# Optimization experiments

Hardware: AMD Instinct MI355X
Metric: run time of the kernel (lower is better)

## Reference

```python
import jax, jax.numpy as jnp
import numpy as np


def setup_inputs() -> dict:
    key = jax.random.key(0)
    k1, k2, k3, k4, k5 = jax.random.split(key, 5)
    B, C, D = 16384, 1000, 2048
    x = jax.random.normal(k1, (B, D), dtype=jnp.float32)
    W = jax.random.normal(k2, (C, D), dtype=jnp.float32) * 0.02  # fc weight
    b = jax.random.normal(k3, (C,), dtype=jnp.float32) * 0.01
    selector_weights = jax.random.normal(k4, (5,), dtype=jnp.float32) * 0.01
    selector_thresholds = jax.random.normal(k5, (5,), dtype=jnp.float32) * 0.01
    ensemble_threshold = jnp.zeros((1,), dtype=jnp.float32)
    return {
        "x": x, "W": W, "b": b,
        "selector_weights": selector_weights,
        "selector_thresholds": selector_thresholds,
        "ensemble_threshold": ensemble_threshold,
    }


def _selector_scores(logits, W):
    # top-2 of raw logits (RLConfM): sorted descending -> top_k(2)
    top2, _ = jax.lax.top_k(logits, 2)
    conf_m = top2[:, 0] - top2[:, 1]
    # geometric margin (RLGeoM): logits normalized by row norms of fc weight
    w_norms = jnp.linalg.norm(W, axis=1)                      # [C]
    norm_logits = logits / (w_norms + 1e-8)[None, :]          # [B, C]
    ntop2, _ = jax.lax.top_k(norm_logits, 2)
    geo_m = ntop2[:, 0] - ntop2[:, 1]
    # softmax-based selectors share one softmax pass
    probs = jax.nn.softmax(logits, axis=1)                    # [B, C]
    sr_max = jnp.max(probs, axis=1)
    doctor = 1.0 - 1.0 / jnp.sum(probs * probs, axis=1)
    neg_entropy = jnp.sum(probs * jnp.log(probs + 1e-10), axis=1)  # = -entropy
    # order matches nn.ModuleList: [SRMax, SRDoctor, SREntropy, RLGeoM, RLConfM]
    return jnp.stack([sr_max, doctor, neg_entropy, geo_m, conf_m], axis=1)  # [B, 5]


def reference(x, W, b, selector_weights, selector_thresholds, ensemble_threshold):
    # base model runs under no_grad in the original
    logits = jax.lax.stop_gradient(jnp.dot(x, W.T) + b)       # [B, C]
    scores = _selector_scores(logits, jax.lax.stop_gradient(W))  # [B, 5]
    indicators = jnp.tanh(scores - selector_thresholds[None, :])  # [B, 5]
    ensemble = jnp.sum(selector_weights[None, :] * indicators, axis=1)  # [B]
    selection_score = jnp.tanh(ensemble - ensemble_threshold[0])
    return (logits, selection_score)
```

## Files before the change

### kernel.cpp

```cpp
#include <hip/hip_runtime.h>
#include <stdint.h>

#define B_ROWS 16384
#define C_COLS 1000
#define D_DIM  2048

typedef __bf16 bf16x8 __attribute__((ext_vector_type(8)));
typedef float  f32x4  __attribute__((ext_vector_type(4)));
typedef unsigned short u16;

__device__ __forceinline__ u16 f2bf(float f) {
  union { float f; uint32_t u; } v; v.f = f;
  return (u16)((v.u + 0x7FFFu + ((v.u >> 16) & 1u)) >> 16);
}

__global__ __launch_bounds__(256)
void prep(const float* __restrict__ W, const float* __restrict__ x,
          u16* __restrict__ Wb, u16* __restrict__ xb, float* __restrict__ norms) {
  const int r = blockIdx.x;
  const int t = threadIdx.x;
  const bool isW = (r < C_COLS);
  const float* src = isW ? (W + (size_t)r * D_DIM)
                         : (x + (size_t)(r - C_COLS) * D_DIM);
  u16* dst = isW ? (Wb + (size_t)r * D_DIM)
                 : (xb + (size_t)(r - C_COLS) * D_DIM);
  const int c = t * 8;
  float4 v0 = *reinterpret_cast<const float4*>(src + c);
  float4 v1 = *reinterpret_cast<const float4*>(src + c + 4);
  uint32_t p0 = (uint32_t)f2bf(v0.x) | ((uint32_t)f2bf(v0.y) << 16);
  uint32_t p1 = (uint32_t)f2bf(v0.z) | ((uint32_t)f2bf(v0.w) << 16);
  uint32_t p2 = (uint32_t)f2bf(v1.x) | ((uint32_t)f2bf(v1.y) << 16);
  uint32_t p3 = (uint32_t)f2bf(v1.z) | ((uint32_t)f2bf(v1.w) << 16);
  const int mask = (r & 7) << 3;
  const int row_id = isW ? r : (r - C_COLS);
  const int m2 = (row_id & 7) << 3;
  (void)mask;
  uint4 val; val.x = p0; val.y = p1; val.z = p2; val.w = p3;
  *reinterpret_cast<uint4*>(dst + (c ^ m2)) = val;
  if (isW) {
    float ss = v0.x*v0.x + v0.y*v0.y + v0.z*v0.z + v0.w*v0.w
             + v1.x*v1.x + v1.y*v1.y + v1.z*v1.z + v1.w*v1.w;
    #pragma unroll
    for (int m = 32; m; m >>= 1) ss += __shfl_xor(ss, m);
    __shared__ float wss[4];
    if ((t & 63) == 0) wss[t >> 6] = ss;
    __syncthreads();
    if (t == 0) norms[r] = sqrtf(wss[0] + wss[1] + wss[2] + wss[3]);
  }
}

#define ABASE(B,H) (((B)*2+(H))*8192)
#define BBASE(B,H) (32768 + ((B)*2+(H))*8192)

#define STAGE_A(BUF,H,KT) { _Pragma("unroll") for (int j_=0;j_<2;++j_){ \
    const char* s_ = (const char*)xb + \
      (((size_t)(m0+(H)*128+j_*64+w*8+(l>>3)))*D_DIM + (KT)*64 + (l&7)*8)*2; \
    u16* d_ = lds + ABASE(BUF,H) + (j_*64 + w*8)*64; \
    __builtin_amdgcn_global_load_lds( \
      (const __attribute__((address_space(1))) void*)s_, \
      (__attribute__((address_space(3))) void*)d_, 16, 0, 0); } }

#define STAGE_B(BUF,H,KT) { _Pragma("unroll") for (int j_=0;j_<2;++j_){ \
    int gr_ = n0+(H)*128+j_*64+w*8+(l>>3); if (gr_ >= C_COLS) gr_ = C_COLS-1; \
    const char* s_ = (const char*)Wb + \
      (((size_t)gr_)*D_DIM + (KT)*64 + (l&7)*8)*2; \
    u16* d_ = lds + BBASE(BUF,H) + (j_*64 + w*8)*64; \
    __builtin_amdgcn_global_load_lds( \
      (const __attribute__((address_space(1))) void*)s_, \
      (__attribute__((address_space(3))) void*)d_, 16, 0, 0); } }

#define PHASE(BUF,MH,NH,STG,VMW) { \
  bf16x8 Af[2][4], Bf[2][2]; \
  _Pragma("unroll") for (int ks=0;ks<2;++ks){ \
    _Pragma("unroll") for (int fr=0;fr<4;++fr){ \
      int ra = wr*64 + fr*16 + (l&15); \
      int ca = (ks*32 + ((l>>4)<<3)) ^ ((ra&7)<<3); \
      Af[ks][fr] = *reinterpret_cast<const bf16x8*>(&lds[ABASE(BUF,MH) + ra*64 + ca]); } \
    _Pragma("unroll") for (int fc=0;fc<2;++fc){ \
      int rb = wcn*32 + fc*16 + (l&15); \
      int cb = (ks*32 + ((l>>4)<<3)) ^ ((rb&7)<<3); \
      Bf[ks][fc] = *reinterpret_cast<const bf16x8*>(&lds[BBASE(BUF,NH) + rb*64 + cb]); } } \
  STG; \
  __builtin_amdgcn_s_barrier(); \
  asm volatile("s_waitcnt lgkmcnt(0)" ::: "memory"); \
  __builtin_amdgcn_sched_barrier(0); \
  __builtin_amdgcn_s_setprio(1); \
  _Pragma("unroll") for (int ks=0;ks<2;++ks) \
    _Pragma("unroll") for (int fr=0;fr<4;++fr) \
      _Pragma("unroll") for (int fc=0;fc<2;++fc) \
        acc[MH][fr][NH][fc] = __builtin_amdgcn_mfma_f32_16x16x32_bf16( \
            Af[ks][fr], Bf[ks][fc], acc[MH][fr][NH][fc], 0, 0, 0); \
  __builtin_amdgcn_s_setprio(0); \
  VMW; \
  __builtin_amdgcn_s_barrier(); }

#define VM4 asm volatile("s_waitcnt vmcnt(4)" ::: "memory")
#define VM0 asm volatile("s_waitcnt vmcnt(0)" ::: "memory")
#define NOP ((void)0)

__global__ __launch_bounds__(512, 2)
void gemm8(const u16* __restrict__ xb, const u16* __restrict__ Wb,
           const float* __restrict__ bias, float* __restrict__ out) {
  __shared__ u16 lds[65536];

  const int bid = blockIdx.x;
  const int swz = (bid & 7) * 32 + (bid >> 3);
  const int tm = swz >> 2, tn = swz & 3;
  const int m0 = tm * 256, n0 = tn * 256;

  const int t = threadIdx.x, w = t >> 6, l = t & 63;
  const int wr = w >> 2, wcn = w & 3;

  f32x4 acc[2][4][2][2];
  #pragma unroll
  for (int a = 0; a < 2; ++a)
    #pragma unroll
    for (int b2 = 0; b2 < 4; ++b2)
      #pragma unroll
      for (int c2 = 0; c2 < 2; ++c2)
        #pragma unroll
        for (int d2 = 0; d2 < 2; ++d2)
          acc[a][b2][c2][d2] = (f32x4){0.f, 0.f, 0.f, 0.f};

  STAGE_A(0,0,0); STAGE_B(0,0,0); STAGE_A(0,1,0); STAGE_B(0,1,0);
  STAGE_A(1,0,1); STAGE_B(1,0,1);
  VM4;
  __builtin_amdgcn_s_barrier();

  for (int it = 0; it < 15; ++it) {
    const int t1k = 2*it + 1, t2k = 2*it + 2, t3k = 2*it + 3;
    PHASE(0,0,0, STAGE_A(1,1,t1k), NOP);
    PHASE(0,0,1, STAGE_B(1,1,t1k), NOP);
    PHASE(0,1,0, STAGE_A(0,0,t2k), NOP);
    PHASE(0,1,1, STAGE_B(0,0,t2k), VM4);
    PHASE(1,0,0, STAGE_A(0,1,t2k), NOP);
    PHASE(1,0,1, STAGE_B(0,1,t2k), NOP);
    PHASE(1,1,0, STAGE_A(1,0,t3k), NOP);
    PHASE(1,1,1, STAGE_B(1,0,t3k), VM4);
  }
  PHASE(0,0,0, STAGE_A(1,1,31), NOP);
  PHASE(0,0,1, STAGE_B(1,1,31), NOP);
  PHASE(0,1,0, NOP, NOP);
  PHASE(0,1,1, NOP, VM0);
  PHASE(1,0,0, NOP, NOP);
  PHASE(1,0,1, NOP, NOP);
  PHASE(1,1,0, NOP, NOP);
  PHASE(1,1,1, NOP, NOP);

  #pragma unroll
  for (int mh = 0; mh < 2; ++mh)
    #pragma unroll
    for (int nh = 0; nh < 2; ++nh)
      #pragma unroll
      for (int fc = 0; fc < 2; ++fc) {
        int col = n0 + nh*128 + wcn*32 + fc*16 + (l & 15);
        if (col < C_COLS) {
          float bv = bias[col];
          #pragma unroll
          for (int fr = 0; fr < 4; ++fr) {
            int row0 = m0 + mh*128 + wr*64 + fr*16 + ((l >> 4) << 2);
            #pragma unroll
            for (int j = 0; j < 4; ++j)
              out[(size_t)(row0 + j) * C_COLS + col] = acc[mh][fr][nh][fc][j] + bv;
          }
        }
      }
}

__global__ __launch_bounds__(256)
void prep_w_fb(const float* __restrict__ W, u16* __restrict__ Wb,
               float* __restrict__ norms) {
  const int r = blockIdx.x;
  const int t = threadIdx.x;
  const float* row = W + (size_t)r * D_DIM;
  const int c = t * 8;
  float4 v0 = *reinterpret_cast<const float4*>(row + c);
  float4 v1 = *reinterpret_cast<const float4*>(row + c + 4);
  float ss = v0.x*v0.x + v0.y*v0.y + v0.z*v0.z + v0.w*v0.w
           + v1.x*v1.x + v1.y*v1.y + v1.z*v1.z + v1.w*v1.w;
  uint32_t p0 = (uint32_t)f2bf(v0.x) | ((uint32_t)f2bf(v0.y) << 16);
  uint32_t p1 = (uint32_t)f2bf(v0.z) | ((uint32_t)f2bf(v0.w) << 16);
  uint32_t p2 = (uint32_t)f2bf(v1.x) | ((uint32_t)f2bf(v1.y) << 16);
  uint32_t p3 = (uint32_t)f2bf(v1.z) | ((uint32_t)f2bf(v1.w) << 16);
  const int mask = (r & 7) << 3;
  uint4 val; val.x = p0; val.y = p1; val.z = p2; val.w = p3;
  *reinterpret_cast<uint4*>(Wb + (size_t)r * D_DIM + (c ^ mask)) = val;
  #pragma unroll
  for (int m = 32; m; m >>= 1) ss += __shfl_xor(ss, m);
  __shared__ float wss[4];
  if ((t & 63) == 0) wss[t >> 6] = ss;
  __syncthreads();
  if (t == 0) norms[r] = sqrtf(wss[0] + wss[1] + wss[2] + wss[3]);
}

__global__ __launch_bounds__(256)
void gemm_fb(const float* __restrict__ x, const u16* __restrict__ Wb,
             const float* __restrict__ bias, float* __restrict__ out) {
  __shared__ u16 lds[(128 + 128) * 64];
  const int bid = blockIdx.x;
  const int cpx = gridDim.x >> 3;
  const int swz = (bid & 7) * cpx + (bid >> 3);
  const int tn = swz & 7, tm = swz >> 3;
  const int m0 = tm * 128, n0 = tn * 128;
  const int t = threadIdx.x, w = t >> 6, l = t & 63;
  const int wr = w >> 1, wc = w & 1;
  f32x4 acc[4][4];
  #pragma unroll
  for (int i = 0; i < 4; ++i)
    #pragma unroll
    for (int j = 0; j < 4; ++j) acc[i][j] = (f32x4){0.f,0.f,0.f,0.f};
  const int ar = w * 32 + (l >> 4);
  const int ac4 = (l & 15) * 4;
  const float* aptr = x + (size_t)(m0 + ar) * D_DIM + ac4;
  for (int k0 = 0; k0 < D_DIM; k0 += 64) {
    #pragma unroll
    for (int i = 0; i < 4; ++i) {
      int ci = w * 4 + i;
      int br = ci * 8 + (l >> 3);
      int wrow = n0 + br; if (wrow >= C_COLS) wrow = C_COLS - 1;
      const char* src = (const char*)Wb + (size_t)wrow * (D_DIM * 2)
                        + k0 * 2 + (l & 7) * 16;
      u16* dst = lds + 128*64 + ci * 512;
      __builtin_amdgcn_global_load_lds(
          (const __attribute__((address_space(1))) void*)src,
          (__attribute__((address_space(3))) void*)dst, 16, 0, 0);
    }
    #pragma unroll
    for (int i = 0; i < 8; ++i) {
      int r = ar + i * 4;
      float4 v = *reinterpret_cast<const float4*>(aptr + (size_t)(i*4)*D_DIM + k0);
      ushort4 h;
      h.x = f2bf(v.x); h.y = f2bf(v.y); h.z = f2bf(v.z); h.w = f2bf(v.w);
      *reinterpret_cast<ushort4*>(&lds[r * 64 + (ac4 ^ ((r & 7) << 3))]) = h;
    }
    __syncthreads();
    #pragma unroll
    for (int kk = 0; kk < 64; kk += 32) {
      const int kg = kk + ((l >> 4) << 3);
      bf16x8 af[4], bfr[4];
      #pragma unroll
      for (int mi = 0; mi < 4; ++mi) {
        int row = wr * 64 + mi * 16 + (l & 15);
        af[mi] = *reinterpret_cast<const bf16x8*>(&lds[row*64 + (kg ^ ((row&7)<<3))]);
      }
      #pragma unroll
      for (int ni = 0; ni < 4; ++ni) {
        int row = wc * 64 + ni * 16 + (l & 15);
        bfr[ni] = *reinterpret_cast<const bf16x8*>(&lds[128*64 + row*64 + (kg ^ ((row&7)<<3))]);
      }
      #pragma unroll
      for (int mi = 0; mi < 4; ++mi)
        #pragma unroll
        for (int ni = 0; ni < 4; ++ni)
          acc[mi][ni] = __builtin_amdgcn_mfma_f32_16x16x32_bf16(
              af[mi], bfr[ni], acc[mi][ni], 0, 0, 0);
    }
    __syncthreads();
  }
  #pragma unroll
  for (int ni = 0; ni < 4; ++ni) {
    int col = n0 + wc * 64 + ni * 16 + (l & 15);
    if (col < C_COLS) {
      float bv = bias[col];
      #pragma unroll
      for (int mi = 0; mi < 4; ++mi) {
        int row0 = m0 + wr * 64 + mi * 16 + ((l >> 4) << 2);
        #pragma unroll
        for (int j = 0; j < 4; ++j)
          out[(size_t)(row0 + j) * C_COLS + col] = acc[mi][ni][j] + bv;
      }
    }
  }
}

__global__ __launch_bounds__(256)
void selector(const float* __restrict__ logits, const float* __restrict__ norms,
              const float* __restrict__ selw, const float* __restrict__ selt,
              const float* __restrict__ ethr, float* __restrict__ out) {
  __shared__ float nrm[C_COLS];
  const int t = threadIdx.x;
  for (int i = t; i < C_COLS; i += 256) nrm[i] = norms[i];
  __syncthreads();

  const int w = t >> 6, l = t & 63;
  const int row = blockIdx.x * 4 + w;
  const float* lp = logits + (size_t)row * C_COLS;

  float lg[16];
  float t1 = -3.4e38f, t2 = -3.4e38f, n1 = -3.4e38f, n2 = -3.4e38f;
  #pragma unroll
  for (int i = 0; i < 16; ++i) {
    int idx = l + i * 64;
    float v = (idx < C_COLS) ? lp[idx] : -3.4e38f;
    lg[i] = v;
    if (v > t1) { t2 = t1; t1 = v; } else if (v > t2) t2 = v;
    float nv = (idx < C_COLS) ? v / (nrm[idx] + 1e-8f) : -3.4e38f;
    if (nv > n1) { n2 = n1; n1 = nv; } else if (nv > n2) n2 = nv;
  }
  #pragma unroll
  for (int m = 1; m < 64; m <<= 1) {
    float o1 = __shfl_xor(t1, m), o2 = __shfl_xor(t2, m);
    if (o1 > t1) { t2 = fmaxf(t1, o2); t1 = o1; } else t2 = fmaxf(t2, o1);
    float p1 = __shfl_xor(n1, m), p2 = __shfl_xor(n2, m);
    if (p1 > n1) { n2 = fmaxf(n1, p2); n1 = p1; } else n2 = fmaxf(n2, p1);
  }
  const float mx = t1;

  float S = 0.f, sq = 0.f;
  float ex[16];
  #pragma unroll
  for (int i = 0; i < 16; ++i) {
    int idx = l + i * 64;
    float e = (idx < C_COLS) ? __expf(lg[i] - mx) : 0.f;
    ex[i] = e; S += e; sq += e * e;
  }
  #pragma unroll
  for (int m = 1; m < 64; m <<= 1) { S += __shfl_xor(S, m); sq += __shfl_xor(sq, m); }

  float ent = 0.f;
  #pragma unroll
  for (int i = 0; i < 16; ++i) {
    int idx = l + i * 64;
    if (idx < C_COLS) {
      float p = ex[i] / S;
      ent += p * __logf(p + 1e-10f);
    }
  }
  #pragma unroll
  for (int m = 1; m < 64; m <<= 1) ent += __shfl_xor(ent, m);

  if (l == 0) {
    float sc0 = 1.f / S;
    float sc1 = 1.f - (S * S) / sq;
    float sc2 = ent;
    float sc3 = n1 - n2;
    float sc4 = t1 - t2;
    float ens = selw[0] * tanhf(sc0 - selt[0])
              + selw[1] * tanhf(sc1 - selt[1])
              + selw[2] * tanhf(sc2 - selt[2])
              + selw[3] * tanhf(sc3 - selt[3])
              + selw[4] * tanhf(sc4 - selt[4]);
    out[row] = tanhf(ens - ethr[0]);
  }
}

extern "C" void kernel_launch(void* const* d_in, const int* in_sizes, int n_in,
                              void* d_out, int out_size, void* d_ws, size_t ws_size,
                              hipStream_t stream) {
  const float* x    = (const float*)d_in[0];
  const float* W    = (const float*)d_in[1];
  const float* b    = (const float*)d_in[2];
  const float* selw = (const float*)d_in[3];
  const float* selt = (const float*)d_in[4];
  const float* ethr = (const float*)d_in[5];
  float* out = (float*)d_out;

  u16*   Wb    = (u16*)d_ws;
  float* norms = (float*)((char*)d_ws + 4096000);
  u16*   xb    = (u16*)((char*)d_ws + 4100096);
  const size_t need = 4100096 + (size_t)B_ROWS * D_DIM * 2;

  if (ws_size >= need) {
    prep<<<C_COLS + B_ROWS, 256, 0, stream>>>(W, x, Wb, xb, norms);
    gemm8<<<256, 512, 0, stream>>>(xb, Wb, b, out);
  } else {
    prep_w_fb<<<C_COLS, 256, 0, stream>>>(W, Wb, norms);
    gemm_fb<<<(B_ROWS / 128) * 8, 256, 0, stream>>>(x, Wb, b, out);
  }
  selector<<<B_ROWS / 4, 256, 0, stream>>>(out, norms, selw, selt, ethr,
                                           out + (size_t)B_ROWS * C_COLS);
}
```

Before: 142.3 us.

## Reuse LDS fragments across GEMM phases and vectorize selector logit loads

```diff
diff --git a/kernel.cpp b/kernel.cpp
--- a/kernel.cpp
+++ b/kernel.cpp
@@ -31,10 +31,8 @@
   uint32_t p1 = (uint32_t)f2bf(v0.z) | ((uint32_t)f2bf(v0.w) << 16);
   uint32_t p2 = (uint32_t)f2bf(v1.x) | ((uint32_t)f2bf(v1.y) << 16);
   uint32_t p3 = (uint32_t)f2bf(v1.z) | ((uint32_t)f2bf(v1.w) << 16);
-  const int mask = (r & 7) << 3;
   const int row_id = isW ? r : (r - C_COLS);
   const int m2 = (row_id & 7) << 3;
-  (void)mask;
   uint4 val; val.x = p0; val.y = p1; val.z = p2; val.w = p3;
   *reinterpret_cast<uint4*>(dst + (c ^ m2)) = val;
   if (isW) {
@@ -69,34 +67,35 @@
       (const __attribute__((address_space(1))) void*)s_, \
       (__attribute__((address_space(3))) void*)d_, 16, 0, 0); } }
 
-#define PHASE(BUF,MH,NH,STG,VMW) { \
-  bf16x8 Af[2][4], Bf[2][2]; \
-  _Pragma("unroll") for (int ks=0;ks<2;++ks){ \
-    _Pragma("unroll") for (int fr=0;fr<4;++fr){ \
-      int ra = wr*64 + fr*16 + (l&15); \
-      int ca = (ks*32 + ((l>>4)<<3)) ^ ((ra&7)<<3); \
-      Af[ks][fr] = *reinterpret_cast<const bf16x8*>(&lds[ABASE(BUF,MH) + ra*64 + ca]); } \
-    _Pragma("unroll") for (int fc=0;fc<2;++fc){ \
-      int rb = wcn*32 + fc*16 + (l&15); \
-      int cb = (ks*32 + ((l>>4)<<3)) ^ ((rb&7)<<3); \
-      Bf[ks][fc] = *reinterpret_cast<const bf16x8*>(&lds[BBASE(BUF,NH) + rb*64 + cb]); } } \
-  STG; \
-  __builtin_amdgcn_s_barrier(); \
-  asm volatile("s_waitcnt lgkmcnt(0)" ::: "memory"); \
-  __builtin_amdgcn_sched_barrier(0); \
+#define READ_A(BUF,MH) { _Pragma("unroll") for (int ks_=0;ks_<2;++ks_) \
+  _Pragma("unroll") for (int fr_=0;fr_<4;++fr_){ \
+    int ra_ = wr*64 + fr_*16 + (l&15); \
+    int ca_ = (ks_*32 + ((l>>4)<<3)) ^ ((ra_&7)<<3); \
+    Acur[ks_][fr_] = *reinterpret_cast<const bf16x8*>( \
+        &lds[ABASE(BUF,MH) + ra_*64 + ca_]); } }
+
+#define READ_B(BUF,NH,DST) { _Pragma("unroll") for (int ks_=0;ks_<2;++ks_) \
+  _Pragma("unroll") for (int fc_=0;fc_<2;++fc_){ \
+    int rb_ = wcn*32 + fc_*16 + (l&15); \
+    int cb_ = (ks_*32 + ((l>>4)<<3)) ^ ((rb_&7)<<3); \
+    DST[ks_][fc_] = *reinterpret_cast<const bf16x8*>( \
+        &lds[BBASE(BUF,NH) + rb_*64 + cb_]); } }
+
+#define MMA(MH,NH,BSRC) { \
   __builtin_amdgcn_s_setprio(1); \
-  _Pragma("unroll") for (int ks=0;ks<2;++ks) \
-    _Pragma("unroll") for (int fr=0;fr<4;++fr) \
-      _Pragma("unroll") for (int fc=0;fc<2;++fc) \
-        acc[MH][fr][NH][fc] = __builtin_amdgcn_mfma_f32_16x16x32_bf16( \
-            Af[ks][fr], Bf[ks][fc], acc[MH][fr][NH][fc], 0, 0, 0); \
-  __builtin_amdgcn_s_setprio(0); \
-  VMW; \
-  __builtin_amdgcn_s_barrier(); }
-
-#define VM4 asm volatile("s_waitcnt vmcnt(4)" ::: "memory")
-#define VM0 asm volatile("s_waitcnt vmcnt(0)" ::: "memory")
-#define NOP ((void)0)
+  _Pragma("unroll") for (int ks_=0;ks_<2;++ks_) \
+    _Pragma("unroll") for (int fr_=0;fr_<4;++fr_) \
+      _Pragma("unroll") for (int fc_=0;fc_<2;++fc_) \
+        acc[MH][fr_][NH][fc_] = __builtin_amdgcn_mfma_f32_16x16x32_bf16( \
+            Acur[ks_][fr_], BSRC[ks_][fc_], acc[MH][fr_][NH][fc_], 0, 0, 0); \
+  __builtin_amdgcn_s_setprio(0); }
+
+#define BAR  __builtin_amdgcn_s_barrier()
+#define LG0  asm volatile("s_waitcnt lgkmcnt(0)" ::: "memory")
+#define LG8  asm volatile("s_waitcnt lgkmcnt(8)" ::: "memory")
+#define SCHB __builtin_amdgcn_sched_barrier(0)
+#define VM4  asm volatile("s_waitcnt vmcnt(4)" ::: "memory")
+#define VM0  asm volatile("s_waitcnt vmcnt(0)" ::: "memory")
 
 __global__ __launch_bounds__(512, 2)
 void gemm8(const u16* __restrict__ xb, const u16* __restrict__ Wb,
@@ -122,30 +121,46 @@
         for (int d2 = 0; d2 < 2; ++d2)
           acc[a][b2][c2][d2] = (f32x4){0.f, 0.f, 0.f, 0.f};
 
+  bf16x8 Acur[2][4], B0c[2][2], B1c[2][2];
+
   STAGE_A(0,0,0); STAGE_B(0,0,0); STAGE_A(0,1,0); STAGE_B(0,1,0);
   STAGE_A(1,0,1); STAGE_B(1,0,1);
   VM4;
-  __builtin_amdgcn_s_barrier();
+  BAR;
 
   for (int it = 0; it < 15; ++it) {
     const int t1k = 2*it + 1, t2k = 2*it + 2, t3k = 2*it + 3;
-    PHASE(0,0,0, STAGE_A(1,1,t1k), NOP);
-    PHASE(0,0,1, STAGE_B(1,1,t1k), NOP);
-    PHASE(0,1,0, STAGE_A(0,0,t2k), NOP);
-    PHASE(0,1,1, STAGE_B(0,0,t2k), VM4);
-    PHASE(1,0,0, STAGE_A(0,1,t2k), NOP);
-    PHASE(1,0,1, STAGE_B(0,1,t2k), NOP);
-    PHASE(1,1,0, STAGE_A(1,0,t3k), NOP);
-    PHASE(1,1,1, STAGE_B(1,0,t3k), VM4);
-  }
-  PHASE(0,0,0, STAGE_A(1,1,31), NOP);
-  PHASE(0,0,1, STAGE_B(1,1,31), NOP);
-  PHASE(0,1,0, NOP, NOP);
-  PHASE(0,1,1, NOP, VM0);
-  PHASE(1,0,0, NOP, NOP);
-  PHASE(1,0,1, NOP, NOP);
-  PHASE(1,1,0, NOP, NOP);
-  PHASE(1,1,1, NOP, NOP);
+    READ_A(0,0); READ_B(0,0,B0c); STAGE_A(1,1,t1k); LG8;
+    BAR; LG0; SCHB; MMA(0,0,B0c); BAR;
+    READ_B(0,1,B1c); STAGE_B(1,1,t1k);
+    BAR; LG0; SCHB; MMA(0,1,B1c); BAR;
+    READ_A(0,1); STAGE_A(0,0,t2k);
+    BAR; LG0; SCHB; MMA(1,1,B1c); BAR;
+    STAGE_B(0,0,t2k);
+    BAR; SCHB; MMA(1,0,B0c); VM4; BAR;
+    READ_A(1,0); READ_B(1,0,B0c); STAGE_A(0,1,t2k); LG8;
+    BAR; LG0; SCHB; MMA(0,0,B0c); BAR;
+    READ_B(1,1,B1c); STAGE_B(0,1,t2k);
+    BAR; LG0; SCHB; MMA(0,1,B1c); BAR;
+    READ_A(1,1); STAGE_A(1,0,t3k);
+    BAR; LG0; SCHB; MMA(1,1,B1c); BAR;
+    STAGE_B(1,0,t3k);
+    BAR; SCHB; MMA(1,0,B0c); VM4; BAR;
+  }
+  READ_A(0,0); READ_B(0,0,B0c); STAGE_A(1,1,31); LG8;
+  BAR; LG0; SCHB; MMA(0,0,B0c); BAR;
+  READ_B(0,1,B1c); STAGE_B(1,1,31);
+  BAR; LG0; SCHB; MMA(0,1,B1c); BAR;
+  READ_A(0,1);
+  BAR; LG0; SCHB; MMA(1,1,B1c); BAR;
+  BAR; SCHB; MMA(1,0,B0c); VM0; BAR;
+  READ_A(1,0); READ_B(1,0,B0c); LG8;
+  BAR; LG0; SCHB; MMA(0,0,B0c); BAR;
+  READ_B(1,1,B1c);
+  BAR; LG0; SCHB; MMA(0,1,B1c); BAR;
+  READ_A(1,1);
+  BAR; LG0; SCHB; MMA(1,1,B1c); BAR;
+  SCHB; MMA(1,0,B0c);
 
   #pragma unroll
   for (int mh = 0; mh < 2; ++mh)
@@ -277,9 +292,13 @@
 void selector(const float* __restrict__ logits, const float* __restrict__ norms,
               const float* __restrict__ selw, const float* __restrict__ selt,
               const float* __restrict__ ethr, float* __restrict__ out) {
-  __shared__ float nrm[C_COLS];
+  __shared__ float nrm[1024];
   const int t = threadIdx.x;
-  for (int i = t; i < C_COLS; i += 256) nrm[i] = norms[i];
+  #pragma unroll
+  for (int i = 0; i < 4; ++i) {
+    int idx = t + i * 256;
+    nrm[idx] = (idx < C_COLS) ? norms[idx] : 1.0f;
+  }
   __syncthreads();
 
   const int w = t >> 6, l = t & 63;
@@ -289,13 +308,19 @@
   float lg[16];
   float t1 = -3.4e38f, t2 = -3.4e38f, n1 = -3.4e38f, n2 = -3.4e38f;
   #pragma unroll
-  for (int i = 0; i < 16; ++i) {
-    int idx = l + i * 64;
-    float v = (idx < C_COLS) ? lp[idx] : -3.4e38f;
-    lg[i] = v;
-    if (v > t1) { t2 = t1; t1 = v; } else if (v > t2) t2 = v;
-    float nv = (idx < C_COLS) ? v / (nrm[idx] + 1e-8f) : -3.4e38f;
-    if (nv > n1) { n2 = n1; n1 = nv; } else if (nv > n2) n2 = nv;
+  for (int i = 0; i < 4; ++i) {
+    float4 v4 = *reinterpret_cast<const float4*>(lp + l * 4 + i * 256);
+    #pragma unroll
+    for (int j = 0; j < 4; ++j) {
+      int idx = l * 4 + i * 256 + j;
+      float raw = (j == 0) ? v4.x : (j == 1) ? v4.y : (j == 2) ? v4.z : v4.w;
+      bool ok = (idx < C_COLS);
+      float v = ok ? raw : -3.4e38f;
+      lg[i * 4 + j] = v;
+      if (v > t1) { t2 = t1; t1 = v; } else if (v > t2) t2 = v;
+      float nv = ok ? raw / (nrm[idx] + 1e-8f) : -3.4e38f;
+      if (nv > n1) { n2 = n1; n1 = nv; } else if (nv > n2) n2 = nv;
+    }
   }
   #pragma unroll
   for (int m = 1; m < 64; m <<= 1) {
@@ -310,8 +335,7 @@
   float ex[16];
   #pragma unroll
   for (int i = 0; i < 16; ++i) {
-    int idx = l + i * 64;
-    float e = (idx < C_COLS) ? __expf(lg[i] - mx) : 0.f;
+    float e = (lg[i] > -1e38f) ? __expf(lg[i] - mx) : 0.f;
     ex[i] = e; S += e; sq += e * e;
   }
   #pragma unroll
@@ -320,8 +344,7 @@
   float ent = 0.f;
   #pragma unroll
   for (int i = 0; i < 16; ++i) {
-    int idx = l + i * 64;
-    if (idx < C_COLS) {
+    if (lg[i] > -1e38f) {
       float p = ex[i] / S;
       ent += p * __logf(p + 1e-10f);
     }
```

New measurement: 133.4 us. 6.3% less time.
